# Kernel tuning notes

Hardware: AMD Instinct MI355X
Metric: run time of the kernel (lower is better)

## Reference

```python
import jax, jax.numpy as jnp
import numpy as np

B, T, D = 4, 2048, 1024

def setup_inputs() -> dict:
    key = jax.random.key(0)
    kx, kq, kk, kv = jax.random.split(key, 4)
    return {
        "vector": jax.random.normal(kx, (B, T, D), dtype=jnp.float32),
        # original uses torch.rand -> uniform [0,1)
        "W_queries": jax.random.uniform(kq, (D, D), dtype=jnp.float32),
        "W_keys": jax.random.uniform(kk, (D, D), dtype=jnp.float32),
        "W_values": jax.random.uniform(kv, (D, D), dtype=jnp.float32),
    }

def reference(vector, W_queries, W_keys, W_values):
    b, num_token, d_out = vector.shape
    queries = vector @ W_queries          # [b, t, d]
    keys = vector @ W_keys                # [b, t, d]
    values = vector @ W_values            # [b, t, d]
    # attention_score: [b, q, k]
    scores = jnp.einsum('bqd,bkd->bqk', queries, keys)
    causal_mask = jnp.triu(jnp.ones((num_token, num_token), dtype=bool), k=1)
    scores = jnp.where(causal_mask[None, :, :], -jnp.inf, scores)
    # NOTE: original uses FLOOR division `//` by sqrt(d_k) -- faithful here.
    inv_sqrt_scale = jnp.asarray(np.sqrt(keys.shape[-1]), dtype=scores.dtype)
    weights = jnp.floor(scores / inv_sqrt_scale)
    # NOTE: original applies softmax over dim=1 (the query axis), not dim=-1.
    weights = jax.nn.softmax(weights, axis=1)
    # dropout rate is 0.0 (eval/deterministic): identity
    context = jnp.einsum('bqk,bkd->bqd', weights, values)
    return context
```

## Files before the change

### kernel.cpp

```cpp
#include <hip/hip_runtime.h>
#include <math.h>

typedef _Float16 half4 __attribute__((ext_vector_type(4)));
typedef _Float16 half8 __attribute__((ext_vector_type(8)));
typedef float f32x4 __attribute__((ext_vector_type(4)));

#define GLD16(gptr, lptr)                                                     \
    __builtin_amdgcn_global_load_lds(                                         \
        (const __attribute__((address_space(1))) unsigned int*)(gptr),        \
        (__attribute__((address_space(3))) unsigned int*)(lptr), 16, 0, 0)

namespace {

constexpr int Bb = 4;
constexpr int Tt = 2048;
constexpr int Dd = 1024;
constexpr int BT = Bb * Tt;
constexpr int NCH = 16;

__device__ inline _Float16 f2h(float f) { return (_Float16)f; }

__global__ __launch_bounds__(256) void convert_x_kernel(
    const float* __restrict__ X, _Float16* __restrict__ Xhi, _Float16* __restrict__ Xlo)
{
    const int idx = (blockIdx.x * 256 + threadIdx.x) * 4;
    const float4 v = *(const float4*)(X + idx);
    const float a[4] = {v.x, v.y, v.z, v.w};
    half4 h, l;
#pragma unroll
    for (int i = 0; i < 4; ++i) {
        h[i] = f2h(a[i]);
        l[i] = f2h(a[i] - (float)h[i]);
    }
    *(half4*)(Xhi + idx) = h;
    *(half4*)(Xlo + idx) = l;
}

__global__ __launch_bounds__(256) void convert_wqk_kernel(
    const float* __restrict__ Wq, const float* __restrict__ Wk,
    _Float16* __restrict__ Wqh, _Float16* __restrict__ Wql,
    _Float16* __restrict__ Wkh, _Float16* __restrict__ Wkl)
{
    const int mat = blockIdx.y;
    const float* W = mat ? Wk : Wq;
    _Float16* Hh = mat ? Wkh : Wqh;
    _Float16* Ll = mat ? Wkl : Wql;
    const int idx = (blockIdx.x * 256 + threadIdx.x) * 4;
    const float4 v = *(const float4*)(W + idx);
    const float a[4] = {v.x, v.y, v.z, v.w};
    half4 h, l;
#pragma unroll
    for (int i = 0; i < 4; ++i) {
        h[i] = f2h(a[i]);
        l[i] = f2h(a[i] - (float)h[i]);
    }
    *(half4*)(Hh + idx) = h;
    *(half4*)(Ll + idx) = l;
}

__global__ __launch_bounds__(256) void convert_wv_kernel(
    const float* __restrict__ Wv, _Float16* __restrict__ WvTh)
{
    __shared__ float tile[64][65];
    const int n0 = blockIdx.x * 64, k0 = blockIdx.y * 64;
    const int tx = threadIdx.x & 63, ty = threadIdx.x >> 6;
#pragma unroll
    for (int i = 0; i < 16; ++i)
        tile[ty + i * 4][tx] = Wv[(size_t)(k0 + ty + i * 4) * Dd + n0 + tx];
    __syncthreads();
#pragma unroll
    for (int i = 0; i < 16; ++i) {
        const float v = tile[tx][ty + i * 4];
        WvTh[(size_t)(n0 + ty + i * 4) * Dd + k0 + tx] = f2h(v);
    }
}

__global__ __launch_bounds__(256) void gt_kernel(
    const _Float16* __restrict__ Wkh, const _Float16* __restrict__ Wkl,
    const _Float16* __restrict__ Wqh, const _Float16* __restrict__ Wql,
    _Float16* __restrict__ GTh, _Float16* __restrict__ GTl)
{
    __shared__ _Float16 Ahl[2][4][512];
    __shared__ _Float16 Bhl[2][4][512];

    const int n0 = blockIdx.x * 64;
    const int m0 = blockIdx.y * 64;
    const int tid = threadIdx.x;
    const int w = tid >> 6, lane = tid & 63;
    const int lr = lane & 15, lq = lane >> 4;
    const int wi = (w >> 1) * 2, wj = (w & 1) * 2;

    f32x4 acc[2][2];
#pragma unroll
    for (int i = 0; i < 2; ++i)
#pragma unroll
        for (int j = 0; j < 2; ++j)
#pragma unroll
            for (int c = 0; c < 4; ++c) acc[i][j][c] = 0.f;

    for (int kk = 0; kk < 1024; kk += 32) {
        __syncthreads();
        {
            const int s = w;
            const size_t ar = (size_t)(m0 + s * 16 + lr) * Dd + kk + lq * 8;
            const size_t br = (size_t)(n0 + s * 16 + lr) * Dd + kk + lq * 8;
            GLD16(Wkh + ar, &Ahl[0][s][0]);
            GLD16(Wkl + ar, &Ahl[1][s][0]);
            GLD16(Wqh + br, &Bhl[0][s][0]);
            GLD16(Wql + br, &Bhl[1][s][0]);
        }
        __syncthreads();
        half8 ah[2], al[2], bh[2], bl[2];
#pragma unroll
        for (int i = 0; i < 2; ++i) {
            ah[i] = *(const half8*)&Ahl[0][wi + i][lane * 8];
            al[i] = *(const half8*)&Ahl[1][wi + i][lane * 8];
        }
#pragma unroll
        for (int j = 0; j < 2; ++j) {
            bh[j] = *(const half8*)&Bhl[0][wj + j][lane * 8];
            bl[j] = *(const half8*)&Bhl[1][wj + j][lane * 8];
        }
#pragma unroll
        for (int i = 0; i < 2; ++i)
#pragma unroll
            for (int j = 0; j < 2; ++j) {
                acc[i][j] = __builtin_amdgcn_mfma_f32_16x16x32_f16(ah[i], bh[j], acc[i][j], 0, 0, 0);
                acc[i][j] = __builtin_amdgcn_mfma_f32_16x16x32_f16(ah[i], bl[j], acc[i][j], 0, 0, 0);
                acc[i][j] = __builtin_amdgcn_mfma_f32_16x16x32_f16(al[i], bh[j], acc[i][j], 0, 0, 0);
            }
    }

#pragma unroll
    for (int i = 0; i < 2; ++i)
#pragma unroll
        for (int r = 0; r < 4; ++r) {
            const int row = m0 + (wi + i) * 16 + lq * 4 + r;
#pragma unroll
            for (int j = 0; j < 2; ++j) {
                const int col = n0 + (wj + j) * 16 + lr;
                const float v = acc[i][j][r];
                const _Float16 h = f2h(v);
                GTh[(size_t)row * Dd + col] = h;
                GTl[(size_t)row * Dd + col] = f2h(v - (float)h);
            }
        }
}

__global__ __launch_bounds__(256) void t_kernel(
    const _Float16* __restrict__ Xhi, const _Float16* __restrict__ Xlo,
    const _Float16* __restrict__ GTh, const _Float16* __restrict__ GTl,
    _Float16* __restrict__ Thi, _Float16* __restrict__ Tlo)
{
    __shared__ _Float16 Ahl[2][8][512];
    __shared__ _Float16 Bhl[2][8][512];

    const int n0 = blockIdx.x * 128;
    const int m0 = blockIdx.y * 128;
    const int tid = threadIdx.x;
    const int w = tid >> 6, lane = tid & 63;
    const int lr = lane & 15, lq = lane >> 4;
    const int wr = (w >> 1) * 4, wc = (w & 1) * 4;

    f32x4 acc[4][4];
#pragma unroll
    for (int i = 0; i < 4; ++i)
#pragma unroll
        for (int j = 0; j < 4; ++j)
#pragma unroll
            for (int c = 0; c < 4; ++c) acc[i][j][c] = 0.f;

    for (int kk = 0; kk < 1024; kk += 32) {
        __syncthreads();
#pragma unroll
        for (int s2 = 0; s2 < 2; ++s2) {
            const int s = w * 2 + s2;
            const size_t ar = (size_t)(m0 + s * 16 + lr) * Dd + kk + lq * 8;
            const size_t br = (size_t)(n0 + s * 16 + lr) * Dd + kk + lq * 8;
            GLD16(Xhi + ar, &Ahl[0][s][0]);
            GLD16(Xlo + ar, &Ahl[1][s][0]);
            GLD16(GTh + br, &Bhl[0][s][0]);
            GLD16(GTl + br, &Bhl[1][s][0]);
        }
        __syncthreads();
        half8 ah[4], al[4], bh[4], bl[4];
#pragma unroll
        for (int i = 0; i < 4; ++i) {
            ah[i] = *(const half8*)&Ahl[0][wr + i][lane * 8];
            al[i] = *(const half8*)&Ahl[1][wr + i][lane * 8];
        }
#pragma unroll
        for (int j = 0; j < 4; ++j) {
            bh[j] = *(const half8*)&Bhl[0][wc + j][lane * 8];
            bl[j] = *(const half8*)&Bhl[1][wc + j][lane * 8];
        }
#pragma unroll
        for (int i = 0; i < 4; ++i)
#pragma unroll
            for (int j = 0; j < 4; ++j) {
                acc[i][j] = __builtin_amdgcn_mfma_f32_16x16x32_f16(ah[i], bh[j], acc[i][j], 0, 0, 0);
                acc[i][j] = __builtin_amdgcn_mfma_f32_16x16x32_f16(ah[i], bl[j], acc[i][j], 0, 0, 0);
                acc[i][j] = __builtin_amdgcn_mfma_f32_16x16x32_f16(al[i], bh[j], acc[i][j], 0, 0, 0);
            }
    }
#pragma unroll
    for (int i = 0; i < 4; ++i)
#pragma unroll
        for (int r = 0; r < 4; ++r) {
            const int row = m0 + (wr + i) * 16 + lq * 4 + r;
#pragma unroll
            for (int j = 0; j < 4; ++j) {
                const int col = n0 + (wc + j) * 16 + lr;
                const float v = acc[i][j][r];
                const _Float16 h = f2h(v);
                Thi[(size_t)row * Dd + col] = h;
                Tlo[(size_t)row * Dd + col] = f2h(v - (float)h);
            }
        }
}

__global__ __launch_bounds__(256) void v_kernel(
    const _Float16* __restrict__ Xhi, const _Float16* __restrict__ WvTh,
    _Float16* __restrict__ Vrow)
{
    __shared__ _Float16 Al[8][512];
    __shared__ _Float16 Bl[8][512];

    const int n0 = blockIdx.x * 128;
    const int m0 = blockIdx.y * 128;
    const int tid = threadIdx.x;
    const int w = tid >> 6, lane = tid & 63;
    const int lr = lane & 15, lq = lane >> 4;
    const int wr = (w >> 1) * 4, wc = (w & 1) * 4;

    f32x4 acc[4][4];
#pragma unroll
    for (int i = 0; i < 4; ++i)
#pragma unroll
        for (int j = 0; j < 4; ++j)
#pragma unroll
            for (int c = 0; c < 4; ++c) acc[i][j][c] = 0.f;

    for (int kk = 0; kk < 1024; kk += 32) {
        __syncthreads();
#pragma unroll
        for (int s2 = 0; s2 < 2; ++s2) {
            const int s = w * 2 + s2;
            GLD16(Xhi + (size_t)(m0 + s * 16 + lr) * Dd + kk + lq * 8, &Al[s][0]);
            GLD16(WvTh + (size_t)(n0 + s * 16 + lr) * Dd + kk + lq * 8, &Bl[s][0]);
        }
        __syncthreads();
        half8 a[4], b2[4];
#pragma unroll
        for (int i = 0; i < 4; ++i) a[i] = *(const half8*)&Al[wr + i][lane * 8];
#pragma unroll
        for (int j = 0; j < 4; ++j) b2[j] = *(const half8*)&Bl[wc + j][lane * 8];
#pragma unroll
        for (int i = 0; i < 4; ++i)
#pragma unroll
            for (int j = 0; j < 4; ++j)
                acc[i][j] = __builtin_amdgcn_mfma_f32_16x16x32_f16(a[i], b2[j], acc[i][j], 0, 0, 0);
    }
#pragma unroll
    for (int i = 0; i < 4; ++i)
#pragma unroll
        for (int r = 0; r < 4; ++r) {
            const int row = m0 + (wr + i) * 16 + lq * 4 + r;
#pragma unroll
            for (int j = 0; j < 4; ++j)
                Vrow[(size_t)row * Dd + n0 + (wc + j) * 16 + lr] = f2h(acc[i][j][r]);
        }
}

__global__ __launch_bounds__(256) void transpose_v_kernel(
    const _Float16* __restrict__ Vrow, const float* __restrict__ Lb,
    _Float16* __restrict__ Vt)
{
    __shared__ _Float16 tile[64][78];
    const int d0 = blockIdx.x * 64, t0 = blockIdx.y * 64, b = blockIdx.z;
    const int tx = threadIdx.x & 63, ty = threadIdx.x >> 6;
#pragma unroll
    for (int i = 0; i < 16; ++i)
        tile[ty + i * 4][tx] = Vrow[((size_t)b * Tt + t0 + ty + i * 4) * Dd + d0 + tx];
    __syncthreads();
    const float sc = Lb[(size_t)b * Tt + t0 + tx];
#pragma unroll
    for (int i = 0; i < 16; ++i) {
        const float v = (float)tile[tx][ty + i * 4] * sc;
        Vt[(size_t)b * Dd * Tt + (size_t)(d0 + ty + i * 4) * Tt + t0 + tx] = f2h(v);
    }
}

__global__ __launch_bounds__(256) void scores_mfma_kernel(
    const _Float16* __restrict__ Thi, const _Float16* __restrict__ Tlo,
    const _Float16* __restrict__ Xhi, const _Float16* __restrict__ Xlo,
    _Float16* __restrict__ P, float* __restrict__ Pm, float* __restrict__ Pl)
{
    const int t = blockIdx.x;
    int byi = (int)((sqrtf(8.f * t + 1.f) - 1.f) * 0.5f);
    if ((byi + 1) * (byi + 2) / 2 <= t) ++byi;
    if (byi * (byi + 1) / 2 > t) --byi;
    const int bxi = t - byi * (byi + 1) / 2;
    const int b = blockIdx.z;
    const int j0 = bxi * 128, q0 = byi * 128;
    _Float16* Pb = P + (size_t)b * Tt * Tt;

    __shared__ _Float16 Ahl[2][8][512];
    __shared__ _Float16 Bhl[2][8][512];
    const _Float16* Th = Thi + (size_t)b * Tt * Dd;
    const _Float16* Tl = Tlo + (size_t)b * Tt * Dd;
    const _Float16* Xh = Xhi + (size_t)b * Tt * Dd;
    const _Float16* Xl = Xlo + (size_t)b * Tt * Dd;

    const int tid = threadIdx.x;
    const int w = tid >> 6, lane = tid & 63;
    const int lr = lane & 15, lq = lane >> 4;
    const int wr = (w >> 1) * 4, wc = (w & 1) * 4;

    f32x4 acc[4][4];
#pragma unroll
    for (int i = 0; i < 4; ++i)
#pragma unroll
        for (int j = 0; j < 4; ++j)
#pragma unroll
            for (int c = 0; c < 4; ++c) acc[i][j][c] = 0.f;

    for (int kk = 0; kk < 1024; kk += 32) {
        __syncthreads();
#pragma unroll
        for (int s2 = 0; s2 < 2; ++s2) {
            const int s = w * 2 + s2;
            const size_t ar = (size_t)(q0 + s * 16 + lr) * Dd + kk + lq * 8;
            const size_t br = (size_t)(j0 + s * 16 + lr) * Dd + kk + lq * 8;
            GLD16(Th + ar, &Ahl[0][s][0]);
            GLD16(Tl + ar, &Ahl[1][s][0]);
            GLD16(Xh + br, &Bhl[0][s][0]);
            GLD16(Xl + br, &Bhl[1][s][0]);
        }
        __syncthreads();
        half8 ah[4], al[4], bh[4], bl[4];
#pragma unroll
        for (int i = 0; i < 4; ++i) {
            ah[i] = *(const half8*)&Ahl[0][wr + i][lane * 8];
            al[i] = *(const half8*)&Ahl[1][wr + i][lane * 8];
        }
#pragma unroll
        for (int j = 0; j < 4; ++j) {
            bh[j] = *(const half8*)&Bhl[0][wc + j][lane * 8];
            bl[j] = *(const half8*)&Bhl[1][wc + j][lane * 8];
        }
#pragma unroll
        for (int i = 0; i < 4; ++i)
#pragma unroll
            for (int j = 0; j < 4; ++j) {
                acc[i][j] = __builtin_amdgcn_mfma_f32_16x16x32_f16(ah[i], bh[j], acc[i][j], 0, 0, 0);
                acc[i][j] = __builtin_amdgcn_mfma_f32_16x16x32_f16(ah[i], bl[j], acc[i][j], 0, 0, 0);
                acc[i][j] = __builtin_amdgcn_mfma_f32_16x16x32_f16(al[i], bh[j], acc[i][j], 0, 0, 0);
            }
    }

    float sv[4][4][4];
#pragma unroll
    for (int i = 0; i < 4; ++i)
#pragma unroll
        for (int r = 0; r < 4; ++r) {
            const int q = q0 + (wr + i) * 16 + lq * 4 + r;
#pragma unroll
            for (int j = 0; j < 4; ++j) {
                const int jg = j0 + (wc + j) * 16 + lr;
                sv[i][j][r] = (jg <= q) ? floorf(acc[i][j][r] * 0.03125f) : -INFINITY;
            }
        }

    float* red  = (float*)&Ahl[0][0][0];
    float* colm = red + 2048;
    __syncthreads();
    for (int e = tid; e < 2048; e += 256) red[e] = -INFINITY;
    __syncthreads();
    const int rowidx = (w * 4 + lq) * 128;
#pragma unroll
    for (int j = 0; j < 4; ++j) {
        const int c = (wc + j) * 16 + lr;
        float lm = -INFINITY;
#pragma unroll
        for (int i = 0; i < 4; ++i)
#pragma unroll
            for (int r = 0; r < 4; ++r) lm = fmaxf(lm, sv[i][j][r]);
        red[rowidx + c] = lm;
    }
    __syncthreads();
    if (tid < 128) {
        float m = -INFINITY;
#pragma unroll
        for (int e = 0; e < 16; ++e) m = fmaxf(m, red[e * 128 + tid]);
        colm[tid] = m;
    }
    __syncthreads();

    float ls[4];
#pragma unroll
    for (int j = 0; j < 4; ++j) {
        const int c = (wc + j) * 16 + lr;
        const float m = colm[c];
        const int jg = j0 + c;
        float s = 0.f;
#pragma unroll
        for (int i = 0; i < 4; ++i)
#pragma unroll
            for (int r = 0; r < 4; ++r) {
                const float e = __expf(sv[i][j][r] - m);
                s += e;
                const int q = q0 + (wr + i) * 16 + lq * 4 + r;
                Pb[(size_t)q * Tt + jg] = f2h(e);
            }
        ls[j] = s;
    }
    __syncthreads();
    for (int e = tid; e < 2048; e += 256) red[e] = 0.f;
    __syncthreads();
#pragma unroll
    for (int j = 0; j < 4; ++j) red[rowidx + (wc + j) * 16 + lr] = ls[j];
    __syncthreads();
    if (tid < 128) {
        float l = 0.f;
#pragma unroll
        for (int e = 0; e < 16; ++e) l += red[e * 128 + tid];
        const size_t o = ((size_t)b * NCH + byi) * Tt + j0 + tid;
        Pm[o] = colm[tid];
        Pl[o] = l;
    }
}

__global__ __launch_bounds__(256) void colstats_merge_kernel(
    const float* __restrict__ Pm, const float* __restrict__ Pl,
    float* __restrict__ Lb, _Float16* __restrict__ Cc)
{
    const int j = blockIdx.x * 256 + threadIdx.x;
    const int b = blockIdx.y;
    const int jt = j >> 7;
    float m = -INFINITY, l = 0.f;
    for (int c = jt; c < NCH; ++c) {
        const size_t pidx = ((size_t)b * NCH + c) * Tt + j;
        const float mi = Pm[pidx];
        if (mi == -INFINITY) continue;
        const float li = Pl[pidx];
        if (mi > m) { l = l * __expf(m - mi) + li; m = mi; }
        else        { l += li * __expf(mi - m); }
    }
    Lb[(size_t)b * Tt + j] = (l > 0.f) ? 1.f / l : 0.f;
    for (int c = jt; c < NCH; ++c) {
        const size_t pidx = ((size_t)b * NCH + c) * Tt + j;
        Cc[pidx] = f2h(__expf(Pm[pidx] - m));
    }
}

__global__ __launch_bounds__(256) void context_mfma_kernel(
    const _Float16* __restrict__ P, const _Float16* __restrict__ Vt,
    const _Float16* __restrict__ Cc, float* __restrict__ Out)
{
    __shared__ _Float16 Al[8][512];
    __shared__ _Float16 Bl[8][512];

    const int bx = blockIdx.x;
    const int by = (int)gridDim.y - 1 - blockIdx.y;
    const int b  = blockIdx.z;
    const int d0 = bx * 128;
    const int q0 = by * 128;
    const _Float16* Pb = P + (size_t)b * Tt * Tt;
    const _Float16* Vb = Vt + (size_t)b * Dd * Tt;
    const _Float16* Ccb = Cc + ((size_t)b * NCH + by) * Tt;
    float* Ob = Out + (size_t)b * Tt * Dd;

    const int tid = threadIdx.x;
    const int w = tid >> 6, lane = tid & 63;
    const int lr = lane & 15, lq = lane >> 4;
    const int wr = (w >> 1) * 4, wc = (w & 1) * 4;

    f32x4 acc[4][4];
#pragma unroll
    for (int i = 0; i < 4; ++i)
#pragma unroll
        for (int j = 0; j < 4; ++j)
#pragma unroll
            for (int c = 0; c < 4; ++c) acc[i][j][c] = 0.f;

    const int kmax = q0 + 128;
    for (int k0 = 0; k0 < kmax; k0 += 32) {
        __syncthreads();
#pragma unroll
        for (int s2 = 0; s2 < 2; ++s2) {
            const int s = w * 2 + s2;
            GLD16(Pb + (size_t)(q0 + s * 16 + lr) * Tt + k0 + lq * 8, &Al[s][0]);
            GLD16(Vb + (size_t)(d0 + s * 16 + lr) * Tt + k0 + lq * 8, &Bl[s][0]);
        }
        __syncthreads();
        const half8 cf = *(const half8*)(Ccb + k0 + lq * 8);
        half8 a[4], b2[4];
#pragma unroll
        for (int i = 0; i < 4; ++i) a[i] = *(const half8*)&Al[wr + i][lane * 8] * cf;
#pragma unroll
        for (int j = 0; j < 4; ++j) b2[j] = *(const half8*)&Bl[wc + j][lane * 8];
#pragma unroll
        for (int i = 0; i < 4; ++i)
#pragma unroll
            for (int j = 0; j < 4; ++j)
                acc[i][j] = __builtin_amdgcn_mfma_f32_16x16x32_f16(a[i], b2[j], acc[i][j], 0, 0, 0);
    }

#pragma unroll
    for (int i = 0; i < 4; ++i)
#pragma unroll
        for (int r = 0; r < 4; ++r) {
            const int row = q0 + (wr + i) * 16 + lq * 4 + r;
#pragma unroll
            for (int j = 0; j < 4; ++j)
                Ob[(size_t)row * Dd + d0 + (wc + j) * 16 + lr] = acc[i][j][r];
        }
}

}

extern "C" void kernel_launch(void* const* d_in, const int* in_sizes, int n_in,
                              void* d_out, int out_size, void* d_ws, size_t ws_size,
                              hipStream_t stream)
{
    const float* X  = (const float*)d_in[0];
    const float* Wq = (const float*)d_in[1];
    const float* Wk = (const float*)d_in[2];
    const float* Wv = (const float*)d_in[3];

    char* ws = (char*)d_ws;
    const size_t MB = 1024 * 1024;
    _Float16* Xhi  = (_Float16*)ws;
    _Float16* Xlo  = (_Float16*)(ws + 16 * MB);
    _Float16* Wqh  = (_Float16*)(ws + 32 * MB);
    _Float16* Wql  = (_Float16*)(ws + 34 * MB);
    _Float16* Wkh  = (_Float16*)(ws + 36 * MB);
    _Float16* Wkl  = (_Float16*)(ws + 38 * MB);
    _Float16* WvTh = (_Float16*)(ws + 40 * MB);
    _Float16* GTh  = (_Float16*)(ws + 44 * MB);
    _Float16* GTl  = (_Float16*)(ws + 46 * MB);
    _Float16* Thi  = (_Float16*)(ws + 48 * MB);
    _Float16* Tlo  = (_Float16*)(ws + 64 * MB);
    _Float16* Vt   = (_Float16*)(ws + 80 * MB);
    _Float16* Vrow = (_Float16*)(ws + 96 * MB);
    _Float16* P    = (_Float16*)(ws + 112 * MB);
    float*    Lb   = (float*)(ws + 176 * MB);
    float*    Pm   = Lb + (size_t)Bb * Tt;
    float*    Pl   = Pm + (size_t)Bb * NCH * Tt;
    _Float16* Cc   = (_Float16*)(Pl + (size_t)Bb * NCH * Tt);
    float*    Out  = (float*)d_out;

    convert_x_kernel<<<BT * Dd / 1024, 256, 0, stream>>>(X, Xhi, Xlo);
    convert_wqk_kernel<<<dim3(Dd * Dd / 1024, 2), 256, 0, stream>>>(Wq, Wk, Wqh, Wql, Wkh, Wkl);
    convert_wv_kernel<<<dim3(16, 16), 256, 0, stream>>>(Wv, WvTh);
    gt_kernel<<<dim3(16, 16), 256, 0, stream>>>(Wkh, Wkl, Wqh, Wql, GTh, GTl);
    t_kernel<<<dim3(8, 64), 256, 0, stream>>>(Xhi, Xlo, GTh, GTl, Thi, Tlo);
    v_kernel<<<dim3(8, 64), 256, 0, stream>>>(Xhi, WvTh, Vrow);
    scores_mfma_kernel<<<dim3(136, 1, Bb), 256, 0, stream>>>(Thi, Tlo, Xhi, Xlo, P, Pm, Pl);
    colstats_merge_kernel<<<dim3(Tt / 256, Bb), 256, 0, stream>>>(Pm, Pl, Lb, Cc);
    transpose_v_kernel<<<dim3(Dd / 64, Tt / 64, Bb), 256, 0, stream>>>(Vrow, Lb, Vt);
    context_mfma_kernel<<<dim3(Dd / 128, Tt / 128, Bb), 256, 0, stream>>>(P, Vt, Cc, Out);
}
```

Measured before the change: 470.8 us.

## Merge weight-convert and T/V projection launches; stage P stores through LDS

The Wq/Wk and Wv conversion kernels are merged into one launch, and the T and V projection GEMMs are merged into one grid whose blocks branch on blockIdx.x. This cuts launch count and lets the two GEMMs share the GPU. In the scores kernel, the exp values are kept in registers and written to a padded LDS tile, then stored to P as coalesced 16-byte rows instead of scattered 2-byte stores. This adds extra syncs and LDS traffic, and the merged GEMM blocks do uneven amounts of work.

Result: slower. 486.7 us (+3.4%).

```diff
diff --git a/kernel.cpp b/kernel.cpp
--- a/kernel.cpp
+++ b/kernel.cpp
@@ -17,6 +17,7 @@
 constexpr int Dd = 1024;
 constexpr int BT = Bb * Tt;
 constexpr int NCH = 16;
+constexpr int PST = 136;
 
 __device__ inline _Float16 f2h(float f) { return (_Float16)f; }
 
@@ -36,42 +37,43 @@
     *(half4*)(Xlo + idx) = l;
 }
 
-__global__ __launch_bounds__(256) void convert_wqk_kernel(
+__global__ __launch_bounds__(256) void convert_w_kernel(
     const float* __restrict__ Wq, const float* __restrict__ Wk,
+    const float* __restrict__ Wv,
     _Float16* __restrict__ Wqh, _Float16* __restrict__ Wql,
-    _Float16* __restrict__ Wkh, _Float16* __restrict__ Wkl)
-{
-    const int mat = blockIdx.y;
-    const float* W = mat ? Wk : Wq;
-    _Float16* Hh = mat ? Wkh : Wqh;
-    _Float16* Ll = mat ? Wkl : Wql;
-    const int idx = (blockIdx.x * 256 + threadIdx.x) * 4;
-    const float4 v = *(const float4*)(W + idx);
-    const float a[4] = {v.x, v.y, v.z, v.w};
-    half4 h, l;
-#pragma unroll
-    for (int i = 0; i < 4; ++i) {
-        h[i] = f2h(a[i]);
-        l[i] = f2h(a[i] - (float)h[i]);
-    }
-    *(half4*)(Hh + idx) = h;
-    *(half4*)(Ll + idx) = l;
-}
-
-__global__ __launch_bounds__(256) void convert_wv_kernel(
-    const float* __restrict__ Wv, _Float16* __restrict__ WvTh)
-{
-    __shared__ float tile[64][65];
-    const int n0 = blockIdx.x * 64, k0 = blockIdx.y * 64;
-    const int tx = threadIdx.x & 63, ty = threadIdx.x >> 6;
-#pragma unroll
-    for (int i = 0; i < 16; ++i)
-        tile[ty + i * 4][tx] = Wv[(size_t)(k0 + ty + i * 4) * Dd + n0 + tx];
-    __syncthreads();
-#pragma unroll
-    for (int i = 0; i < 16; ++i) {
-        const float v = tile[tx][ty + i * 4];
-        WvTh[(size_t)(n0 + ty + i * 4) * Dd + k0 + tx] = f2h(v);
+    _Float16* __restrict__ Wkh, _Float16* __restrict__ Wkl,
+    _Float16* __restrict__ WvTh)
+{
+    const int y = blockIdx.y;
+    if (y < 2) {
+        const float* W = y ? Wk : Wq;
+        _Float16* Hh = y ? Wkh : Wqh;
+        _Float16* Ll = y ? Wkl : Wql;
+        const int idx = (blockIdx.x * 256 + threadIdx.x) * 4;
+        const float4 v = *(const float4*)(W + idx);
+        const float a[4] = {v.x, v.y, v.z, v.w};
+        half4 h, l;
+#pragma unroll
+        for (int i = 0; i < 4; ++i) {
+            h[i] = f2h(a[i]);
+            l[i] = f2h(a[i] - (float)h[i]);
+        }
+        *(half4*)(Hh + idx) = h;
+        *(half4*)(Ll + idx) = l;
+    } else {
+        if (blockIdx.x >= 256) return;
+        __shared__ float tile[64][65];
+        const int n0 = (blockIdx.x & 15) * 64, k0 = (blockIdx.x >> 4) * 64;
+        const int tx = threadIdx.x & 63, ty = threadIdx.x >> 6;
+#pragma unroll
+        for (int i = 0; i < 16; ++i)
+            tile[ty + i * 4][tx] = Wv[(size_t)(k0 + ty + i * 4) * Dd + n0 + tx];
+        __syncthreads();
+#pragma unroll
+        for (int i = 0; i < 16; ++i) {
+            const float v = tile[tx][ty + i * 4];
+            WvTh[(size_t)(n0 + ty + i * 4) * Dd + k0 + tx] = f2h(v);
+        }
     }
 }
 
@@ -147,15 +149,17 @@
         }
 }
 
-__global__ __launch_bounds__(256) void t_kernel(
+__global__ __launch_bounds__(256) void tv_kernel(
     const _Float16* __restrict__ Xhi, const _Float16* __restrict__ Xlo,
     const _Float16* __restrict__ GTh, const _Float16* __restrict__ GTl,
-    _Float16* __restrict__ Thi, _Float16* __restrict__ Tlo)
-{
-    __shared__ _Float16 Ahl[2][8][512];
-    __shared__ _Float16 Bhl[2][8][512];
-
-    const int n0 = blockIdx.x * 128;
+    const _Float16* __restrict__ WvTh,
+    _Float16* __restrict__ Thi, _Float16* __restrict__ Tlo,
+    _Float16* __restrict__ Vrow)
+{
+    __shared__ _Float16 smem[16384];
+
+    const bool isT = blockIdx.x < 8;
+    const int n0 = (blockIdx.x & 7) * 128;
     const int m0 = blockIdx.y * 128;
     const int tid = threadIdx.x;
     const int w = tid >> 6, lane = tid & 63;
@@ -170,106 +174,85 @@
 #pragma unroll
             for (int c = 0; c < 4; ++c) acc[i][j][c] = 0.f;
 
-    for (int kk = 0; kk < 1024; kk += 32) {
-        __syncthreads();
-#pragma unroll
-        for (int s2 = 0; s2 < 2; ++s2) {
-            const int s = w * 2 + s2;
-            const size_t ar = (size_t)(m0 + s * 16 + lr) * Dd + kk + lq * 8;
-            const size_t br = (size_t)(n0 + s * 16 + lr) * Dd + kk + lq * 8;
-            GLD16(Xhi + ar, &Ahl[0][s][0]);
-            GLD16(Xlo + ar, &Ahl[1][s][0]);
-            GLD16(GTh + br, &Bhl[0][s][0]);
-            GLD16(GTl + br, &Bhl[1][s][0]);
-        }
-        __syncthreads();
-        half8 ah[4], al[4], bh[4], bl[4];
-#pragma unroll
-        for (int i = 0; i < 4; ++i) {
-            ah[i] = *(const half8*)&Ahl[0][wr + i][lane * 8];
-            al[i] = *(const half8*)&Ahl[1][wr + i][lane * 8];
-        }
-#pragma unroll
-        for (int j = 0; j < 4; ++j) {
-            bh[j] = *(const half8*)&Bhl[0][wc + j][lane * 8];
-            bl[j] = *(const half8*)&Bhl[1][wc + j][lane * 8];
+    if (isT) {
+        for (int kk = 0; kk < 1024; kk += 32) {
+            __syncthreads();
+#pragma unroll
+            for (int s2 = 0; s2 < 2; ++s2) {
+                const int s = w * 2 + s2;
+                const size_t ar = (size_t)(m0 + s * 16 + lr) * Dd + kk + lq * 8;
+                const size_t br = (size_t)(n0 + s * 16 + lr) * Dd + kk + lq * 8;
+                GLD16(Xhi + ar, smem + s * 512);
+                GLD16(Xlo + ar, smem + 4096 + s * 512);
+                GLD16(GTh + br, smem + 8192 + s * 512);
+                GLD16(GTl + br, smem + 12288 + s * 512);
+            }
+            __syncthreads();
+            half8 ah[4], al[4], bh[4], bl[4];
+#pragma unroll
+            for (int i = 0; i < 4; ++i) {
+                ah[i] = *(const half8*)&smem[(wr + i) * 512 + lane * 8];
+                al[i] = *(const half8*)&smem[4096 + (wr + i) * 512 + lane * 8];
+            }
+#pragma unroll
+            for (int j = 0; j < 4; ++j) {
+                bh[j] = *(const half8*)&smem[8192 + (wc + j) * 512 + lane * 8];
+                bl[j] = *(const half8*)&smem[12288 + (wc + j) * 512 + lane * 8];
+            }
+#pragma unroll
+            for (int i = 0; i < 4; ++i)
+#pragma unroll
+                for (int j = 0; j < 4; ++j) {
+                    acc[i][j] = __builtin_amdgcn_mfma_f32_16x16x32_f16(ah[i], bh[j], acc[i][j], 0, 0, 0);
+                    acc[i][j] = __builtin_amdgcn_mfma_f32_16x16x32_f16(ah[i], bl[j], acc[i][j], 0, 0, 0);
+                    acc[i][j] = __builtin_amdgcn_mfma_f32_16x16x32_f16(al[i], bh[j], acc[i][j], 0, 0, 0);
+                }
         }
 #pragma unroll
         for (int i = 0; i < 4; ++i)
 #pragma unroll
-            for (int j = 0; j < 4; ++j) {
-                acc[i][j] = __builtin_amdgcn_mfma_f32_16x16x32_f16(ah[i], bh[j], acc[i][j], 0, 0, 0);
-                acc[i][j] = __builtin_amdgcn_mfma_f32_16x16x32_f16(ah[i], bl[j], acc[i][j], 0, 0, 0);
-                acc[i][j] = __builtin_amdgcn_mfma_f32_16x16x32_f16(al[i], bh[j], acc[i][j], 0, 0, 0);
-            }
-    }
-#pragma unroll
-    for (int i = 0; i < 4; ++i)
-#pragma unroll
-        for (int r = 0; r < 4; ++r) {
-            const int row = m0 + (wr + i) * 16 + lq * 4 + r;
-#pragma unroll
-            for (int j = 0; j < 4; ++j) {
-                const int col = n0 + (wc + j) * 16 + lr;
-                const float v = acc[i][j][r];
-                const _Float16 h = f2h(v);
-                Thi[(size_t)row * Dd + col] = h;
-                Tlo[(size_t)row * Dd + col] = f2h(v - (float)h);
-            }
-        }
-}
-
-__global__ __launch_bounds__(256) void v_kernel(
-    const _Float16* __restrict__ Xhi, const _Float16* __restrict__ WvTh,
-    _Float16* __restrict__ Vrow)
-{
-    __shared__ _Float16 Al[8][512];
-    __shared__ _Float16 Bl[8][512];
-
-    const int n0 = blockIdx.x * 128;
-    const int m0 = blockIdx.y * 128;
-    const int tid = threadIdx.x;
-    const int w = tid >> 6, lane = tid & 63;
-    const int lr = lane & 15, lq = lane >> 4;
-    const int wr = (w >> 1) * 4, wc = (w & 1) * 4;
-
-    f32x4 acc[4][4];
-#pragma unroll
-    for (int i = 0; i < 4; ++i)
-#pragma unroll
-        for (int j = 0; j < 4; ++j)
-#pragma unroll
-            for (int c = 0; c < 4; ++c) acc[i][j][c] = 0.f;
-
-    for (int kk = 0; kk < 1024; kk += 32) {
-        __syncthreads();
-#pragma unroll
-        for (int s2 = 0; s2 < 2; ++s2) {
-            const int s = w * 2 + s2;
-            GLD16(Xhi + (size_t)(m0 + s * 16 + lr) * Dd + kk + lq * 8, &Al[s][0]);
-            GLD16(WvTh + (size_t)(n0 + s * 16 + lr) * Dd + kk + lq * 8, &Bl[s][0]);
-        }
-        __syncthreads();
-        half8 a[4], b2[4];
-#pragma unroll
-        for (int i = 0; i < 4; ++i) a[i] = *(const half8*)&Al[wr + i][lane * 8];
-#pragma unroll
-        for (int j = 0; j < 4; ++j) b2[j] = *(const half8*)&Bl[wc + j][lane * 8];
+            for (int r = 0; r < 4; ++r) {
+                const int row = m0 + (wr + i) * 16 + lq * 4 + r;
+#pragma unroll
+                for (int j = 0; j < 4; ++j) {
+                    const int col = n0 + (wc + j) * 16 + lr;
+                    const float v = acc[i][j][r];
+                    const _Float16 h = f2h(v);
+                    Thi[(size_t)row * Dd + col] = h;
+                    Tlo[(size_t)row * Dd + col] = f2h(v - (float)h);
+                }
+            }
+    } else {
+        for (int kk = 0; kk < 1024; kk += 32) {
+            __syncthreads();
+#pragma unroll
+            for (int s2 = 0; s2 < 2; ++s2) {
+                const int s = w * 2 + s2;
+                GLD16(Xhi + (size_t)(m0 + s * 16 + lr) * Dd + kk + lq * 8, smem + s * 512);
+                GLD16(WvTh + (size_t)(n0 + s * 16 + lr) * Dd + kk + lq * 8, smem + 8192 + s * 512);
+            }
+            __syncthreads();
+            half8 a[4], b2[4];
+#pragma unroll
+            for (int i = 0; i < 4; ++i) a[i] = *(const half8*)&smem[(wr + i) * 512 + lane * 8];
+#pragma unroll
+            for (int j = 0; j < 4; ++j) b2[j] = *(const half8*)&smem[8192 + (wc + j) * 512 + lane * 8];
+#pragma unroll
+            for (int i = 0; i < 4; ++i)
+#pragma unroll
+                for (int j = 0; j < 4; ++j)
+                    acc[i][j] = __builtin_amdgcn_mfma_f32_16x16x32_f16(a[i], b2[j], acc[i][j], 0, 0, 0);
+        }
 #pragma unroll
         for (int i = 0; i < 4; ++i)
 #pragma unroll
-            for (int j = 0; j < 4; ++j)
-                acc[i][j] = __builtin_amdgcn_mfma_f32_16x16x32_f16(a[i], b2[j], acc[i][j], 0, 0, 0);
-    }
-#pragma unroll
-    for (int i = 0; i < 4; ++i)
-#pragma unroll
-        for (int r = 0; r < 4; ++r) {
-            const int row = m0 + (wr + i) * 16 + lq * 4 + r;
-#pragma unroll
-            for (int j = 0; j < 4; ++j)
-                Vrow[(size_t)row * Dd + n0 + (wc + j) * 16 + lr] = f2h(acc[i][j][r]);
-        }
+            for (int r = 0; r < 4; ++r) {
+                const int row = m0 + (wr + i) * 16 + lq * 4 + r;
+#pragma unroll
+                for (int j = 0; j < 4; ++j)
+                    Vrow[(size_t)row * Dd + n0 + (wc + j) * 16 + lr] = f2h(acc[i][j][r]);
+            }
+    }
 }
 
 __global__ __launch_bounds__(256) void transpose_v_kernel(
@@ -305,8 +288,7 @@
     const int j0 = bxi * 128, q0 = byi * 128;
     _Float16* Pb = P + (size_t)b * Tt * Tt;
 
-    __shared__ _Float16 Ahl[2][8][512];
-    __shared__ _Float16 Bhl[2][8][512];
+    __shared__ _Float16 smem[16384];
     const _Float16* Th = Thi + (size_t)b * Tt * Dd;
     const _Float16* Tl = Tlo + (size_t)b * Tt * Dd;
     const _Float16* Xh = Xhi + (size_t)b * Tt * Dd;
@@ -332,22 +314,22 @@
             const int s = w * 2 + s2;
             const size_t ar = (size_t)(q0 + s * 16 + lr) * Dd + kk + lq * 8;
             const size_t br = (size_t)(j0 + s * 16 + lr) * Dd + kk + lq * 8;
-            GLD16(Th + ar, &Ahl[0][s][0]);
-            GLD16(Tl + ar, &Ahl[1][s][0]);
-            GLD16(Xh + br, &Bhl[0][s][0]);
-            GLD16(Xl + br, &Bhl[1][s][0]);
+            GLD16(Th + ar, smem + s * 512);
+            GLD16(Tl + ar, smem + 4096 + s * 512);
+            GLD16(Xh + br, smem + 8192 + s * 512);
+            GLD16(Xl + br, smem + 12288 + s * 512);
         }
         __syncthreads();
         half8 ah[4], al[4], bh[4], bl[4];
 #pragma unroll
         for (int i = 0; i < 4; ++i) {
-            ah[i] = *(const half8*)&Ahl[0][wr + i][lane * 8];
-            al[i] = *(const half8*)&Ahl[1][wr + i][lane * 8];
+            ah[i] = *(const half8*)&smem[(wr + i) * 512 + lane * 8];
+            al[i] = *(const half8*)&smem[4096 + (wr + i) * 512 + lane * 8];
         }
 #pragma unroll
         for (int j = 0; j < 4; ++j) {
-            bh[j] = *(const half8*)&Bhl[0][wc + j][lane * 8];
-            bl[j] = *(const half8*)&Bhl[1][wc + j][lane * 8];
+            bh[j] = *(const half8*)&smem[8192 + (wc + j) * 512 + lane * 8];
+            bl[j] = *(const half8*)&smem[12288 + (wc + j) * 512 + lane * 8];
         }
 #pragma unroll
         for (int i = 0; i < 4; ++i)
@@ -372,7 +354,7 @@
             }
         }
 
-    float* red  = (float*)&Ahl[0][0][0];
+    float* red  = (float*)smem;
     float* colm = red + 2048;
     __syncthreads();
     for (int e = tid; e < 2048; e += 256) red[e] = -INFINITY;
@@ -402,16 +384,14 @@
     for (int j = 0; j < 4; ++j) {
         const int c = (wc + j) * 16 + lr;
         const float m = colm[c];
-        const int jg = j0 + c;
         float s = 0.f;
 #pragma unroll
         for (int i = 0; i < 4; ++i)
 #pragma unroll
             for (int r = 0; r < 4; ++r) {
                 const float e = __expf(sv[i][j][r] - m);
+                sv[i][j][r] = e;
                 s += e;
-                const int q = q0 + (wr + i) * 16 + lq * 4 + r;
-                Pb[(size_t)q * Tt + jg] = f2h(e);
             }
         ls[j] = s;
     }
@@ -428,6 +408,35 @@
         const size_t o = ((size_t)b * NCH + byi) * Tt + j0 + tid;
         Pm[o] = colm[tid];
         Pl[o] = l;
+    }
+
+    _Float16* pt = smem;
+    const int tr = tid >> 4;
+    const int tc = (tid & 15) * 8;
+#pragma unroll
+    for (int half = 0; half < 2; ++half) {
+        __syncthreads();
+        if ((w >> 1) == half) {
+#pragma unroll
+            for (int i = 0; i < 4; ++i) {
+                const int lrow = i * 16 + lq * 4;
+#pragma unroll
+                for (int j = 0; j < 4; ++j) {
+                    const int c = (wc + j) * 16 + lr;
+#pragma unroll
+                    for (int r = 0; r < 4; ++r)
+                        pt[(lrow + r) * PST + c] = f2h(sv[i][j][r]);
+                }
+            }
+        }
+        __syncthreads();
+#pragma unroll
+        for (int rr = 0; rr < 4; ++rr) {
+            const int lrow = rr * 16 + tr;
+            const int q = q0 + half * 64 + lrow;
+            const half8 v8 = *(const half8*)&pt[lrow * PST + tc];
+            *(half8*)(Pb + (size_t)q * Tt + j0 + tc) = v8;
+        }
     }
 }
 
@@ -552,11 +561,10 @@
     float*    Out  = (float*)d_out;
 
     convert_x_kernel<<<BT * Dd / 1024, 256, 0, stream>>>(X, Xhi, Xlo);
-    convert_wqk_kernel<<<dim3(Dd * Dd / 1024, 2), 256, 0, stream>>>(Wq, Wk, Wqh, Wql, Wkh, Wkl);
-    convert_wv_kernel<<<dim3(16, 16), 256, 0, stream>>>(Wv, WvTh);
+    convert_w_kernel<<<dim3(Dd * Dd / 1024, 3), 256, 0, stream>>>(
+        Wq, Wk, Wv, Wqh, Wql, Wkh, Wkl, WvTh);
     gt_kernel<<<dim3(16, 16), 256, 0, stream>>>(Wkh, Wkl, Wqh, Wql, GTh, GTl);
-    t_kernel<<<dim3(8, 64), 256, 0, stream>>>(Xhi, Xlo, GTh, GTl, Thi, Tlo);
-    v_kernel<<<dim3(8, 64), 256, 0, stream>>>(Xhi, WvTh, Vrow);
+    tv_kernel<<<dim3(16, 64), 256, 0, stream>>>(Xhi, Xlo, GTh, GTl, WvTh, Thi, Tlo, Vrow);
     scores_mfma_kernel<<<dim3(136, 1, Bb), 256, 0, stream>>>(Thi, Tlo, Xhi, Xlo, P, Pm, Pl);
     colstats_merge_kernel<<<dim3(Tt / 256, Bb), 256, 0, stream>>>(Pm, Pl, Lb, Cc);
     transpose_v_kernel<<<dim3(Dd / 64, Tt / 64, Bb), 256, 0, stream>>>(Vrow, Lb, Vt);
```
